# Kernel tuning notes

Measured on AMD Instinct MI355X. Metric: run time of the kernel, lower is better.

The kernel has to match this reference:

```python
import jax, jax.numpy as jnp
import numpy as np

NUM_HEADS = 16
HEAD_DIM = 64
ROT_DIM = 64
NUM_EXPERTS = 8
TOP_K = 2
EPS = 1e-6


def _rms_norm(x, w):
    var = jnp.mean(x * x, axis=-1, keepdims=True)
    return w * x * jax.lax.rsqrt(var + EPS)


def _rotate_half(x):
    h = x.shape[-1] // 2
    return jnp.concatenate((-x[..., h:], x[..., :h]), axis=-1)


def _rotary_cos_sin(seq_len, rot_dim, dtype):
    inv_freq = 1.0 / (10000.0 ** (jnp.arange(0, rot_dim, 2, dtype=jnp.float32) / rot_dim))
    t = jnp.arange(seq_len, dtype=jnp.float32)
    freqs = t[:, None] * inv_freq[None, :]            # [S, rot/2]
    emb = jnp.concatenate((freqs, freqs), axis=-1)    # [S, rot]
    return jnp.cos(emb).astype(dtype), jnp.sin(emb).astype(dtype)


def setup_inputs() -> dict:
    key = jax.random.key(0)
    ks = jax.random.split(key, 10)
    B, S, D, H, E = 2, 2048, 1024, 2048, NUM_EXPERTS
    s = lambda fan: 1.0 / np.sqrt(fan)
    return {
        "x": jax.random.normal(ks[0], (B, S, D), jnp.float32),
        "norm1_w": jnp.ones((D,), jnp.float32),
        "norm2_w": jnp.ones((D,), jnp.float32),
        "qkv_w": jax.random.normal(ks[1], (3 * D, D), jnp.float32) * s(D),
        "qkv_b": jnp.zeros((3 * D,), jnp.float32),
        "out_w": jax.random.normal(ks[2], (D, D), jnp.float32) * s(D),
        "out_b": jnp.zeros((D,), jnp.float32),
        "gate_w": jax.random.normal(ks[3], (E, D), jnp.float32) * s(D),
        "w1": jax.random.normal(ks[4], (E, H, D), jnp.float32) * s(D),
        "b1": jnp.zeros((E, H), jnp.float32),
        "w2": jax.random.normal(ks[5], (E, H, D), jnp.float32) * s(D),
        "b2": jnp.zeros((E, H), jnp.float32),
        "w3": jax.random.normal(ks[6], (E, D, H), jnp.float32) * s(H),
        "b3": jnp.zeros((E, D), jnp.float32),
    }


def _attention(x, qkv_w, qkv_b, out_w, out_b):
    B, S, D = x.shape
    qkv = x @ qkv_w.T + qkv_b                                  # [B,S,3D]
    qkv = qkv.reshape(B, S, 3, NUM_HEADS, HEAD_DIM)
    qkv = jnp.transpose(qkv, (2, 0, 3, 1, 4))                  # [3,B,H,S,Dh]
    q, k, v = qkv[0], qkv[1], qkv[2]
    cos, sin = _rotary_cos_sin(S, ROT_DIM, x.dtype)            # [S,rot]
    cos = cos[None, None]
    sin = sin[None, None]

    def rope(t):
        tr = t[..., :ROT_DIM]
        return jnp.concatenate((tr * cos + _rotate_half(tr) * sin, t[..., ROT_DIM:]), axis=-1)

    q, k = rope(q), rope(k)
    scale = HEAD_DIM ** -0.5
    scores = jnp.einsum("bhqd,bhkd->bhqk", q, k) * scale
    attn = jax.nn.softmax(scores, axis=-1)
    out = jnp.einsum("bhqk,bhkd->bhqd", attn, v)
    out = jnp.transpose(out, (0, 2, 1, 3)).reshape(B, S, D)
    return out @ out_w.T + out_b


def _sparse_moe(x, gate_w, w1, b1, w2, b2, w3, b3):
    logits = x @ gate_w.T                                      # [B,S,E]
    top_vals, top_idx = jax.lax.top_k(logits, TOP_K)
    gate_scores = jax.nn.softmax(top_vals, axis=-1)            # [B,S,k]
    # combined per-expert weight [B,S,E]
    comb = jnp.sum(jax.nn.one_hot(top_idx, NUM_EXPERTS, dtype=x.dtype)
                   * gate_scores[..., None], axis=-2)
    out = jnp.zeros_like(x)
    for e in range(NUM_EXPERTS):  # small fixed expert count; matches dense all-expert compute
        h = jax.nn.silu(x @ w1[e].T + b1[e]) * (x @ w2[e].T + b2[e])
        y = h @ w3[e].T + b3[e]
        out = out + y * comb[..., e:e + 1]
    return out


def reference(x, norm1_w, norm2_w, qkv_w, qkv_b, out_w, out_b,
              gate_w, w1, b1, w2, b2, w3, b3):
    x = x + _attention(_rms_norm(x, norm1_w), qkv_w, qkv_b, out_w, out_b)
    x = x + _sparse_moe(_rms_norm(x, norm2_w), gate_w, w1, b1, w2, b2, w3, b3)
    return x
```

## Files before the change

### kernel.cpp

```cpp
#include <hip/hip_runtime.h>
#include <stdint.h>

typedef unsigned short u16;
typedef __attribute__((ext_vector_type(4))) float f32x4;
typedef __attribute__((ext_vector_type(8))) short bf16x8;

#define MFMA16(a, b, c) __builtin_amdgcn_mfma_f32_16x16x32_bf16((a), (b), (c), 0, 0, 0)

__device__ __forceinline__ float bu2f(u16 u) {
  union { unsigned int i; float f; } c; c.i = ((unsigned int)u) << 16; return c.f;
}
__device__ __forceinline__ u16 f2bu(float f) {
  union { float f; unsigned int i; } c; c.f = f;
  unsigned int x = c.i;
  return (u16)((x + 0x7FFFu + ((x >> 16) & 1u)) >> 16);
}

typedef const __attribute__((address_space(1))) void GVoid;
typedef __attribute__((address_space(3))) void LVoid;

__device__ __forceinline__ void gl_lds16(const void* g, void* l) {
  __builtin_amdgcn_global_load_lds((GVoid*)(uintptr_t)g, (LVoid*)(uintptr_t)l, 16, 0, 0);
}

struct __align__(16) bf8pack { u16 v[8]; };
struct __align__(8) bf4pack { u16 v[4]; };

__global__ __launch_bounds__(256) void f2b_kernel(const float* __restrict__ in,
                                                  u16* __restrict__ out, int n8) {
  int i = blockIdx.x * 256 + threadIdx.x;
  if (i >= n8) return;
  const f32x4* in4 = (const f32x4*)in;
  f32x4 a = in4[i * 2], b = in4[i * 2 + 1];
  bf8pack p;
  p.v[0] = f2bu(a[0]); p.v[1] = f2bu(a[1]); p.v[2] = f2bu(a[2]); p.v[3] = f2bu(a[3]);
  p.v[4] = f2bu(b[0]); p.v[5] = f2bu(b[1]); p.v[6] = f2bu(b[2]); p.v[7] = f2bu(b[3]);
  ((bf8pack*)out)[i] = p;
}

__global__ __launch_bounds__(256) void wsplit3_kernel(const float* __restrict__ w,
                                                      u16* __restrict__ out) {
  int i = blockIdx.x * 256 + threadIdx.x;
  int n = i >> 7, k0 = (i & 127) * 8;
  const f32x4* p = (const f32x4*)(w + (size_t)n * 1024 + k0);
  f32x4 a = p[0], b = p[1];
  float f[8] = {a[0], a[1], a[2], a[3], b[0], b[1], b[2], b[3]};
  bf8pack hi, lo;
#pragma unroll
  for (int t = 0; t < 8; ++t) {
    hi.v[t] = f2bu(f[t]);
    lo.v[t] = f2bu(f[t] - bu2f(hi.v[t]));
  }
  u16* o = out + (size_t)n * 3072 + k0;
  *(bf8pack*)o = hi;
  *(bf8pack*)(o + 1024) = hi;
  *(bf8pack*)(o + 2048) = lo;
}

__global__ __launch_bounds__(256) void asplit3_kernel(const float* __restrict__ a,
                                                      u16* __restrict__ out) {
  int i = blockIdx.x * 256 + threadIdx.x;
  int n = i >> 7, k0 = (i & 127) * 8;
  const f32x4* p = (const f32x4*)(a + (size_t)n * 1024 + k0);
  f32x4 x = p[0], y = p[1];
  float f[8] = {x[0], x[1], x[2], x[3], y[0], y[1], y[2], y[3]};
  bf8pack hi, lo;
#pragma unroll
  for (int t = 0; t < 8; ++t) {
    hi.v[t] = f2bu(f[t]);
    lo.v[t] = f2bu(f[t] - bu2f(hi.v[t]));
  }
  u16* o = out + (size_t)n * 3072 + k0;
  *(bf8pack*)o = hi;
  *(bf8pack*)(o + 1024) = lo;
  *(bf8pack*)(o + 2048) = hi;
}

__global__ __launch_bounds__(256) void rmsnorm3_kernel(const float* __restrict__ x,
                                                       const float* __restrict__ w,
                                                       u16* __restrict__ out) {
  int row = blockIdx.x;
  int tid = threadIdx.x;
  const f32x4* xr = (const f32x4*)(x + (size_t)row * 1024);
  f32x4 v = xr[tid];
  float ss = v[0] * v[0] + v[1] * v[1] + v[2] * v[2] + v[3] * v[3];
#pragma unroll
  for (int off = 32; off; off >>= 1) ss += __shfl_xor(ss, off);
  __shared__ float part[4];
  if ((tid & 63) == 0) part[tid >> 6] = ss;
  __syncthreads();
  float rs = rsqrtf((part[0] + part[1] + part[2] + part[3]) * (1.0f / 1024.0f) + 1e-6f);
  const f32x4* w4 = (const f32x4*)w;
  f32x4 wv = w4[tid];
  float f[4] = {v[0] * rs * wv[0], v[1] * rs * wv[1], v[2] * rs * wv[2], v[3] * rs * wv[3]};
  bf4pack hi, lo;
#pragma unroll
  for (int t = 0; t < 4; ++t) {
    hi.v[t] = f2bu(f[t]);
    lo.v[t] = f2bu(f[t] - bu2f(hi.v[t]));
  }
  u16* o = out + (size_t)row * 3072;
  ((bf4pack*)o)[tid] = hi;
  ((bf4pack*)(o + 1024))[tid] = lo;
  ((bf4pack*)(o + 2048))[tid] = hi;
}

__global__ __launch_bounds__(256) void rmsnorm_kernel(const float* __restrict__ x,
                                                      const float* __restrict__ w,
                                                      u16* __restrict__ out) {
  int row = blockIdx.x;
  int tid = threadIdx.x;
  const f32x4* xr = (const f32x4*)(x + (size_t)row * 1024);
  f32x4 v = xr[tid];
  float ss = v[0] * v[0] + v[1] * v[1] + v[2] * v[2] + v[3] * v[3];
#pragma unroll
  for (int off = 32; off; off >>= 1) ss += __shfl_xor(ss, off);
  __shared__ float part[4];
  if ((tid & 63) == 0) part[tid >> 6] = ss;
  __syncthreads();
  float rs = rsqrtf((part[0] + part[1] + part[2] + part[3]) * (1.0f / 1024.0f) + 1e-6f);
  const f32x4* w4 = (const f32x4*)w;
  f32x4 wv = w4[tid];
  bf4pack o;
  o.v[0] = f2bu(v[0] * rs * wv[0]);
  o.v[1] = f2bu(v[1] * rs * wv[1]);
  o.v[2] = f2bu(v[2] * rs * wv[2]);
  o.v[3] = f2bu(v[3] * rs * wv[3]);
  ((bf4pack*)out)[(size_t)row * 256 + tid] = o;
}

template <int MODE>
__global__ __launch_bounds__(256, 2) void gemm_kernel(
    const u16* __restrict__ A, const u16* __restrict__ B1g, const u16* __restrict__ B2g,
    const float* __restrict__ bias1, const float* __restrict__ bias2,
    void* __restrict__ outp, const float* __restrict__ resid, int N, int K,
    const int* __restrict__ counts, const int* __restrict__ opad,
    const int* __restrict__ slot_token, const float* __restrict__ slot_weight) {
  constexpr bool DUAL = (MODE == 2);
  const int tid = threadIdx.x;
  const int lane = tid & 63;
  const int wid = tid >> 6;
  const int wr = wid >> 1, wc = wid & 1;
  const int n0 = blockIdx.x * 128;
  const int mt = blockIdx.y;
  const int e = (MODE >= 2) ? blockIdx.z : 0;
  int m0;
  if (MODE >= 2) {
    int cnt = counts[e];
    if (mt * 128 >= cnt) return;
    m0 = opad[e] + mt * 128;
  } else {
    m0 = mt * 128;
  }
  const u16* B1 = B1g + ((MODE >= 2) ? (size_t)e * (size_t)N * (size_t)K : (size_t)0);
  const u16* B2 = DUAL ? (B2g + (size_t)e * (size_t)N * (size_t)K) : nullptr;
  const float* bb1 = bias1 + ((MODE >= 2) ? e * N : 0);
  const float* bb2 = DUAL ? (bias2 + e * N) : nullptr;

  __shared__ u16 smem[(DUAL ? 3 : 2) * 128 * 64];
  u16* As = smem;
  u16* Bs = smem + 128 * 64;
  u16* B2s = smem + 2 * 128 * 64;

  const f32x4 zero4 = {0.f, 0.f, 0.f, 0.f};
  f32x4 acc[4][4], acc2[4][4];
#pragma unroll
  for (int mi = 0; mi < 4; ++mi)
#pragma unroll
    for (int ni = 0; ni < 4; ++ni) {
      acc[mi][ni] = zero4;
      if constexpr (DUAL) acc2[mi][ni] = zero4;
    }

  const int rsel = lane & 15;
  const int ksel = lane >> 4;

  for (int k0 = 0; k0 < K; k0 += 64) {
    if (k0) __syncthreads();
#pragma unroll
    for (int i = 0; i < 4; ++i) {
      int c = tid + i * 256;
      int row = c >> 3;
      int col = (c & 7) * 8;
      size_t arow;
      if constexpr (MODE == 2) arow = (size_t)slot_token[m0 + row];
      else arow = (size_t)(m0 + row);
      gl_lds16(A + arow * (size_t)K + k0 + col, As + c * 8);
      gl_lds16(B1 + (size_t)(n0 + row) * K + k0 + col, Bs + c * 8);
      if constexpr (DUAL) gl_lds16(B2 + (size_t)(n0 + row) * K + k0 + col, B2s + c * 8);
    }
    __syncthreads();
    const u16* Aw = As + (wr * 64) * 64;
    const u16* Bw = Bs + (wc * 64) * 64;
    const u16* B2w = B2s + (wc * 64) * 64;
#pragma unroll
    for (int ks = 0; ks < 2; ++ks) {
      int ko = ks * 32 + ksel * 8;
      bf16x8 a[4], b[4];
#pragma unroll
      for (int mi = 0; mi < 4; ++mi) a[mi] = *(const bf16x8*)(Aw + (mi * 16 + rsel) * 64 + ko);
#pragma unroll
      for (int ni = 0; ni < 4; ++ni) b[ni] = *(const bf16x8*)(Bw + (ni * 16 + rsel) * 64 + ko);
#pragma unroll
      for (int mi = 0; mi < 4; ++mi)
#pragma unroll
        for (int ni = 0; ni < 4; ++ni) acc[mi][ni] = MFMA16(a[mi], b[ni], acc[mi][ni]);
      if constexpr (DUAL) {
        bf16x8 b2[4];
#pragma unroll
        for (int ni = 0; ni < 4; ++ni) b2[ni] = *(const bf16x8*)(B2w + (ni * 16 + rsel) * 64 + ko);
#pragma unroll
        for (int mi = 0; mi < 4; ++mi)
#pragma unroll
          for (int ni = 0; ni < 4; ++ni) acc2[mi][ni] = MFMA16(a[mi], b2[ni], acc2[mi][ni]);
      }
    }
  }

#pragma unroll
  for (int mi = 0; mi < 4; ++mi) {
#pragma unroll
    for (int j = 0; j < 4; ++j) {
      int gm = m0 + wr * 64 + mi * 16 + ksel * 4 + j;
#pragma unroll
      for (int ni = 0; ni < 4; ++ni) {
        int gn = n0 + wc * 64 + ni * 16 + rsel;
        float v = acc[mi][ni][j];
        if constexpr (MODE == 0) {
          ((float*)outp)[(size_t)gm * N + gn] = v + bb1[gn];
        } else if constexpr (MODE == 1) {
          ((float*)outp)[(size_t)gm * N + gn] = v + bb1[gn] + resid[(size_t)gm * N + gn];
        } else if constexpr (MODE == 2) {
          float v1 = v + bb1[gn];
          float v2 = acc2[mi][ni][j] + bb2[gn];
          float hv = (v1 / (1.f + __expf(-v1))) * v2;
          ((u16*)outp)[(size_t)gm * N + gn] = f2bu(hv);
        } else {
          int tok = slot_token[gm];
          float w = slot_weight[gm];
          atomicAdd(((float*)outp) + (size_t)tok * N + gn, (v + bb1[gn]) * w);
        }
      }
    }
  }
}

__global__ __launch_bounds__(256) void rope_split_kernel(
    const float* __restrict__ qkv, u16* __restrict__ qhp, u16* __restrict__ qlp,
    u16* __restrict__ khp, u16* __restrict__ klp, u16* __restrict__ vhp,
    u16* __restrict__ vlp) {
  int idx = blockIdx.x * 256 + threadIdx.x;
  int hd = idx & 63;
  int s = (idx >> 6) & 2047;
  int bh = idx >> 17;
  int b = bh >> 4, h = bh & 15;
  size_t base = (size_t)(b * 2048 + s) * 3072 + (size_t)h * 64;
  float qv = qkv[base + hd];
  float qp = qkv[base + (hd ^ 32)];
  float kv = qkv[base + 1024 + hd];
  float kp = qkv[base + 1024 + (hd ^ 32)];
  float vv = qkv[base + 2048 + hd];
  int j = hd & 31;
  double invf = exp((double)j * (-9.210340371976184 / 32.0));
  double ang = (double)s * invf;
  const double twopi = 6.283185307179586;
  double r = ang - twopi * floor(ang / twopi);
  float sn, c;
  sincosf((float)r, &sn, &c);
  float qo = (hd < 32) ? (qv * c - qp * sn) : (qv * c + qp * sn);
  float ko = (hd < 32) ? (kv * c - kp * sn) : (kv * c + kp * sn);
  u16 qh = f2bu(qo), kh = f2bu(ko), vh = f2bu(vv);
  qhp[idx] = qh; qlp[idx] = f2bu(qo - bu2f(qh));
  khp[idx] = kh; klp[idx] = f2bu(ko - bu2f(kh));
  vhp[idx] = vh; vlp[idx] = f2bu(vv - bu2f(vh));
}

__global__ __launch_bounds__(256, 2) void flash_kernel(
    const u16* __restrict__ qhp, const u16* __restrict__ qlp, const u16* __restrict__ khp,
    const u16* __restrict__ klp, const u16* __restrict__ vhp, const u16* __restrict__ vlp,
    float* __restrict__ attn_out) {
  int qblk = blockIdx.x, bh = blockIdx.y;
  int tid = threadIdx.x, lane = tid & 63, wid = tid >> 6;
  const int rsel = lane & 15, ksel = lane >> 4;
  const size_t bhbase = (size_t)bh * 2048 * 64;
  __shared__ u16 Ksh[64 * 64], Ksl[64 * 64];
  __shared__ u16 Vsh[64 * 64], Vsl[64 * 64];
  __shared__ u16 Psh[4][16 * 64], Psl[4][16 * 64];
  int qr0 = qblk * 64 + wid * 16;
  bf16x8 qfh[2], qfl[2];
#pragma unroll
  for (int ks = 0; ks < 2; ++ks) {
    size_t qoff = bhbase + (size_t)(qr0 + rsel) * 64 + ks * 32 + ksel * 8;
    qfh[ks] = *(const bf16x8*)(qhp + qoff);
    qfl[ks] = *(const bf16x8*)(qlp + qoff);
  }

  const f32x4 zero4 = {0.f, 0.f, 0.f, 0.f};
  f32x4 po[4];
  float m_i[4], l_i[4];
#pragma unroll
  for (int i = 0; i < 4; ++i) { po[i] = zero4; m_i[i] = -1e30f; l_i[i] = 0.f; }

  for (int kv0 = 0; kv0 < 2048; kv0 += 64) {
    __syncthreads();
#pragma unroll
    for (int i = 0; i < 2; ++i) {
      int c = tid + i * 256;
      gl_lds16(khp + bhbase + (size_t)kv0 * 64 + c * 8, Ksh + c * 8);
      gl_lds16(klp + bhbase + (size_t)kv0 * 64 + c * 8, Ksl + c * 8);
    }
#pragma unroll
    for (int i = 0; i < 2; ++i) {
      int c = tid + i * 256;
      int r = c >> 3, col0 = (c & 7) * 8;
      bf16x8 a = *(const bf16x8*)(vhp + bhbase + (size_t)(kv0 + r) * 64 + col0);
      bf16x8 bl = *(const bf16x8*)(vlp + bhbase + (size_t)(kv0 + r) * 64 + col0);
#pragma unroll
      for (int jj = 0; jj < 8; ++jj) {
        Vsh[(col0 + jj) * 64 + r] = (u16)a[jj];
        Vsl[(col0 + jj) * 64 + r] = (u16)bl[jj];
      }
    }
    __syncthreads();

    f32x4 sa[4] = {zero4, zero4, zero4, zero4};
#pragma unroll
    for (int ks = 0; ks < 2; ++ks) {
      int ko = ks * 32 + ksel * 8;
#pragma unroll
      for (int ni = 0; ni < 4; ++ni) {
        bf16x8 kbh = *(const bf16x8*)(Ksh + (ni * 16 + rsel) * 64 + ko);
        bf16x8 kbl = *(const bf16x8*)(Ksl + (ni * 16 + rsel) * 64 + ko);
        sa[ni] = MFMA16(qfh[ks], kbh, sa[ni]);
        sa[ni] = MFMA16(qfl[ks], kbh, sa[ni]);
        sa[ni] = MFMA16(qfh[ks], kbl, sa[ni]);
      }
    }
    const float scale = 0.125f;
    float corr[4];
#pragma unroll
    for (int i = 0; i < 4; ++i) {
      float t = sa[0][i] * scale;
      t = fmaxf(t, sa[1][i] * scale);
      t = fmaxf(t, sa[2][i] * scale);
      t = fmaxf(t, sa[3][i] * scale);
#pragma unroll
      for (int off = 1; off < 16; off <<= 1) t = fmaxf(t, __shfl_xor(t, off));
      float mn = fmaxf(m_i[i], t);
      corr[i] = __expf(m_i[i] - mn);
      m_i[i] = mn;
    }
    float rsum[4] = {0.f, 0.f, 0.f, 0.f};
#pragma unroll
    for (int ni = 0; ni < 4; ++ni)
#pragma unroll
      for (int i = 0; i < 4; ++i) {
        float p = __expf(sa[ni][i] * scale - m_i[i]);
        rsum[i] += p;
        u16 ph = f2bu(p);
        Psh[wid][(ksel * 4 + i) * 64 + ni * 16 + rsel] = ph;
        Psl[wid][(ksel * 4 + i) * 64 + ni * 16 + rsel] = f2bu(p - bu2f(ph));
      }
#pragma unroll
    for (int i = 0; i < 4; ++i) {
      float t = rsum[i];
#pragma unroll
      for (int off = 1; off < 16; off <<= 1) t += __shfl_xor(t, off);
      l_i[i] = l_i[i] * corr[i] + t;
    }
#pragma unroll
    for (int nh = 0; nh < 4; ++nh)
#pragma unroll
      for (int i = 0; i < 4; ++i) po[nh][i] *= corr[i];
    __syncthreads();
#pragma unroll
    for (int ks = 0; ks < 2; ++ks) {
      int ko = ks * 32 + ksel * 8;
      bf16x8 pfh = *(const bf16x8*)(&Psh[wid][rsel * 64 + ko]);
      bf16x8 pfl = *(const bf16x8*)(&Psl[wid][rsel * 64 + ko]);
#pragma unroll
      for (int nh = 0; nh < 4; ++nh) {
        bf16x8 vbh = *(const bf16x8*)(Vsh + (nh * 16 + rsel) * 64 + ko);
        bf16x8 vbl = *(const bf16x8*)(Vsl + (nh * 16 + rsel) * 64 + ko);
        po[nh] = MFMA16(pfh, vbh, po[nh]);
        po[nh] = MFMA16(pfl, vbh, po[nh]);
        po[nh] = MFMA16(pfh, vbl, po[nh]);
      }
    }
  }
  int b = bh >> 4, h = bh & 15;
#pragma unroll
  for (int i = 0; i < 4; ++i) {
    float inv = 1.0f / l_i[i];
    int row = qr0 + ksel * 4 + i;
    size_t obase = (size_t)(b * 2048 + row) * 1024 + (size_t)h * 64;
#pragma unroll
    for (int nh = 0; nh < 4; ++nh) attn_out[obase + nh * 16 + rsel] = po[nh][i] * inv;
  }
}

__global__ __launch_bounds__(256) void gate_kernel(const float* __restrict__ xres,
                                                   const float* __restrict__ n2w,
                                                   const float* __restrict__ gw,
                                                   int* __restrict__ tok_e, float* __restrict__ tok_w,
                                                   int* __restrict__ counts) {
  int token = blockIdx.x * 4 + (threadIdx.x >> 6);
  int lane = threadIdx.x & 63;
  const f32x4* xr = (const f32x4*)(xres + (size_t)token * 1024);
  f32x4 xv[4];
  float ss = 0.f;
#pragma unroll
  for (int i = 0; i < 4; ++i) {
    xv[i] = xr[lane * 4 + i];
    ss += xv[i][0] * xv[i][0] + xv[i][1] * xv[i][1] + xv[i][2] * xv[i][2] + xv[i][3] * xv[i][3];
  }
#pragma unroll
  for (int off = 32; off; off >>= 1) ss += __shfl_xor(ss, off);
  float rs = rsqrtf(ss * (1.0f / 1024.0f) + 1e-6f);
  const f32x4* w4 = (const f32x4*)n2w;
#pragma unroll
  for (int i = 0; i < 4; ++i) {
    f32x4 wv = w4[lane * 4 + i];
    xv[i][0] *= rs * wv[0]; xv[i][1] *= rs * wv[1]; xv[i][2] *= rs * wv[2]; xv[i][3] *= rs * wv[3];
  }
  float lg[8];
#pragma unroll
  for (int ee = 0; ee < 8; ++ee) {
    const f32x4* g4 = (const f32x4*)(gw + ee * 1024);
    float a = 0.f;
#pragma unroll
    for (int i = 0; i < 4; ++i) {
      f32x4 g = g4[lane * 4 + i];
      a += xv[i][0] * g[0] + xv[i][1] * g[1] + xv[i][2] * g[2] + xv[i][3] * g[3];
    }
#pragma unroll
    for (int off = 32; off; off >>= 1) a += __shfl_xor(a, off);
    lg[ee] = a;
  }
  if (lane == 0) {
    int i1 = 0; float v1 = lg[0];
#pragma unroll
    for (int ee = 1; ee < 8; ++ee) if (lg[ee] > v1) { v1 = lg[ee]; i1 = ee; }
    int i2 = -1; float v2 = -3e38f;
#pragma unroll
    for (int ee = 0; ee < 8; ++ee) if (ee != i1 && lg[ee] > v2) { v2 = lg[ee]; i2 = ee; }
    float s2 = 1.f / (1.f + __expf(v1 - v2));
    float s1 = 1.f - s2;
    tok_e[token * 2] = i1; tok_e[token * 2 + 1] = i2;
    tok_w[token * 2] = s1; tok_w[token * 2 + 1] = s2;
    atomicAdd(&counts[i1], 1); atomicAdd(&counts[i2], 1);
  }
}

__global__ void init_kernel(int* counts, int* cursor, int* slot_token, float* slot_weight) {
  int i = blockIdx.x * 256 + threadIdx.x;
  if (i < 8) { counts[i] = 0; cursor[i] = 0; }
  if (i < 10240) { slot_token[i] = 0; slot_weight[i] = 0.f; }
}

__global__ void scan_kernel(const int* counts, int* opad) {
  if (threadIdx.x == 0) {
    int off = 0;
    for (int e = 0; e < 8; ++e) { opad[e] = off; off += ((counts[e] + 127) >> 7) << 7; }
  }
}

__global__ __launch_bounds__(256) void assign_kernel(const int* __restrict__ tok_e,
                                                     const float* __restrict__ tok_w,
                                                     const int* __restrict__ opad, int* cursor,
                                                     int* __restrict__ slot_token,
                                                     float* __restrict__ slot_weight) {
  int t = blockIdx.x * 256 + threadIdx.x;
#pragma unroll
  for (int j = 0; j < 2; ++j) {
    int e = tok_e[t * 2 + j];
    int pos = atomicAdd(&cursor[e], 1);
    slot_token[opad[e] + pos] = t;
    slot_weight[opad[e] + pos] = tok_w[t * 2 + j];
  }
}

extern "C" void kernel_launch(void* const* d_in, const int* in_sizes, int n_in, void* d_out,
                              int out_size, void* d_ws, size_t ws_size, hipStream_t stream) {
  const float* x = (const float*)d_in[0];
  const float* n1w = (const float*)d_in[1];
  const float* n2w = (const float*)d_in[2];
  const float* qkv_w = (const float*)d_in[3];
  const float* qkv_b = (const float*)d_in[4];
  const float* out_w = (const float*)d_in[5];
  const float* out_b = (const float*)d_in[6];
  const float* gate_w = (const float*)d_in[7];
  const float* w1 = (const float*)d_in[8];
  const float* b1 = (const float*)d_in[9];
  const float* w2 = (const float*)d_in[10];
  const float* b2 = (const float*)d_in[11];
  const float* w3 = (const float*)d_in[12];
  const float* b3 = (const float*)d_in[13];
  float* out = (float*)d_out;

  const size_t MB = 1024 * 1024;
  char* ws = (char*)d_ws;
  char* R0 = ws;
  char* R1 = ws + 96 * MB;
  char* R2 = R1 + 44 * MB;
  char* R3 = R2 + 16 * MB;
  char* R4 = R3 + 8 * MB;
  if ((size_t)(165 * MB) > ws_size) return;

  float* qkvbuf = (float*)R0;
  u16* qhp = (u16*)(R0 + 48 * MB);
  u16* qlp = (u16*)(R0 + 56 * MB);
  u16* khp = (u16*)(R0 + 64 * MB);
  u16* klp = (u16*)(R0 + 72 * MB);
  u16* vhp = (u16*)(R0 + 80 * MB);
  u16* vlp = (u16*)(R0 + 88 * MB);
  u16* w1b = (u16*)R0;
  u16* w2b = (u16*)(R0 + 32 * MB);
  u16* w3b = (u16*)(R0 + 64 * MB);
  u16* xn3 = (u16*)R1;
  u16* qkvw3 = (u16*)(R1 + 24 * MB);
  u16* attn3 = (u16*)R1;
  u16* hbuf = (u16*)R1;
  float* attnout = (float*)R2;
  u16* xn_moe = (u16*)R2;
  u16* outw3 = (u16*)R3;
  int* tok_e = (int*)R4;
  float* tok_w = (float*)(R4 + 64 * 1024);
  int* counts = (int*)(R4 + 128 * 1024);
  int* cursor = (int*)(R4 + 132 * 1024);
  int* opad = (int*)(R4 + 136 * 1024);
  int* slot_token = (int*)(R4 + 192 * 1024);
  float* slot_weight = (float*)(R4 + 256 * 1024);

  rmsnorm3_kernel<<<4096, 256, 0, stream>>>(x, n1w, xn3);
  wsplit3_kernel<<<1536, 256, 0, stream>>>(qkv_w, qkvw3);
  wsplit3_kernel<<<512, 256, 0, stream>>>(out_w, outw3);
  gemm_kernel<0><<<dim3(24, 32, 1), 256, 0, stream>>>(xn3, qkvw3, nullptr, qkv_b, nullptr, qkvbuf,
                                                      nullptr, 3072, 3072, nullptr, nullptr,
                                                      nullptr, nullptr);
  rope_split_kernel<<<16384, 256, 0, stream>>>(qkvbuf, qhp, qlp, khp, klp, vhp, vlp);
  flash_kernel<<<dim3(32, 32, 1), 256, 0, stream>>>(qhp, qlp, khp, klp, vhp, vlp, attnout);
  f2b_kernel<<<8192, 256, 0, stream>>>(w1, w1b, 2097152);
  f2b_kernel<<<8192, 256, 0, stream>>>(w2, w2b, 2097152);
  f2b_kernel<<<8192, 256, 0, stream>>>(w3, w3b, 2097152);
  asplit3_kernel<<<2048, 256, 0, stream>>>(attnout, attn3);
  gemm_kernel<1><<<dim3(8, 32, 1), 256, 0, stream>>>(attn3, outw3, nullptr, out_b, nullptr, out, x,
                                                     1024, 3072, nullptr, nullptr, nullptr, nullptr);
  rmsnorm_kernel<<<4096, 256, 0, stream>>>(out, n2w, xn_moe);
  init_kernel<<<40, 256, 0, stream>>>(counts, cursor, slot_token, slot_weight);
  gate_kernel<<<1024, 256, 0, stream>>>(out, n2w, gate_w, tok_e, tok_w, counts);
  scan_kernel<<<1, 64, 0, stream>>>(counts, opad);
  assign_kernel<<<16, 256, 0, stream>>>(tok_e, tok_w, opad, cursor, slot_token, slot_weight);
  gemm_kernel<2><<<dim3(16, 32, 8), 256, 0, stream>>>(xn_moe, w1b, w2b, b1, b2, hbuf, nullptr, 2048,
                                                      1024, counts, opad, slot_token, slot_weight);
  gemm_kernel<3><<<dim3(8, 32, 8), 256, 0, stream>>>(hbuf, w3b, nullptr, b3, nullptr, out, nullptr,
                                                     1024, 2048, counts, opad, slot_token,
                                                     slot_weight);
}
```

Measured before the change: 1.170 ms.

## Swizzle flash-attention LDS tiles, raise occupancy, and prioritize MFMA sections

Applies an XOR swizzle to the K, V and P shared-memory tiles in the flash attention kernel so the 16-byte fragment reads and transposed V writes avoid LDS bank conflicts. K tiles loaded through global_load_lds are swizzled on the source address, so each LDS slot holds the element its read index expects. It also raises the launch bound to 3 blocks per SM and wraps the MFMA loops in s_setprio. The extra occupancy may cause register spills, and the swizzle adds index arithmetic to every access.

```diff
diff --git a/kernel.cpp b/kernel.cpp
--- a/kernel.cpp
+++ b/kernel.cpp
@@ -22,6 +22,8 @@
 __device__ __forceinline__ void gl_lds16(const void* g, void* l) {
   __builtin_amdgcn_global_load_lds((GVoid*)(uintptr_t)g, (LVoid*)(uintptr_t)l, 16, 0, 0);
 }
+
+__device__ __forceinline__ int swz(int row) { return ((row ^ (row >> 3)) & 7) << 3; }
 
 struct __align__(16) bf8pack { u16 v[8]; };
 struct __align__(8) bf4pack { u16 v[4]; };
@@ -275,7 +277,7 @@
   vhp[idx] = vh; vlp[idx] = f2bu(vv - bu2f(vh));
 }
 
-__global__ __launch_bounds__(256, 2) void flash_kernel(
+__global__ __launch_bounds__(256, 3) void flash_kernel(
     const u16* __restrict__ qhp, const u16* __restrict__ qlp, const u16* __restrict__ khp,
     const u16* __restrict__ klp, const u16* __restrict__ vhp, const u16* __restrict__ vlp,
     float* __restrict__ attn_out) {
@@ -306,8 +308,9 @@
 #pragma unroll
     for (int i = 0; i < 2; ++i) {
       int c = tid + i * 256;
-      gl_lds16(khp + bhbase + (size_t)kv0 * 64 + c * 8, Ksh + c * 8);
-      gl_lds16(klp + bhbase + (size_t)kv0 * 64 + c * 8, Ksl + c * 8);
+      int srcoff = (c * 8) ^ swz(c >> 3);
+      gl_lds16(khp + bhbase + (size_t)kv0 * 64 + srcoff, Ksh + c * 8);
+      gl_lds16(klp + bhbase + (size_t)kv0 * 64 + srcoff, Ksl + c * 8);
     }
 #pragma unroll
     for (int i = 0; i < 2; ++i) {
@@ -317,25 +320,31 @@
       bf16x8 bl = *(const bf16x8*)(vlp + bhbase + (size_t)(kv0 + r) * 64 + col0);
 #pragma unroll
       for (int jj = 0; jj < 8; ++jj) {
-        Vsh[(col0 + jj) * 64 + r] = (u16)a[jj];
-        Vsl[(col0 + jj) * 64 + r] = (u16)bl[jj];
+        int d = col0 + jj;
+        int widx = (d * 64 + r) ^ swz(d);
+        Vsh[widx] = (u16)a[jj];
+        Vsl[widx] = (u16)bl[jj];
       }
     }
     __syncthreads();
 
     f32x4 sa[4] = {zero4, zero4, zero4, zero4};
+    __builtin_amdgcn_s_setprio(1);
 #pragma unroll
     for (int ks = 0; ks < 2; ++ks) {
       int ko = ks * 32 + ksel * 8;
 #pragma unroll
       for (int ni = 0; ni < 4; ++ni) {
-        bf16x8 kbh = *(const bf16x8*)(Ksh + (ni * 16 + rsel) * 64 + ko);
-        bf16x8 kbl = *(const bf16x8*)(Ksl + (ni * 16 + rsel) * 64 + ko);
+        int row = ni * 16 + rsel;
+        int idx = (row * 64 + ko) ^ swz(row);
+        bf16x8 kbh = *(const bf16x8*)(Ksh + idx);
+        bf16x8 kbl = *(const bf16x8*)(Ksl + idx);
         sa[ni] = MFMA16(qfh[ks], kbh, sa[ni]);
         sa[ni] = MFMA16(qfl[ks], kbh, sa[ni]);
         sa[ni] = MFMA16(qfh[ks], kbl, sa[ni]);
       }
     }
+    __builtin_amdgcn_s_setprio(0);
     const float scale = 0.125f;
     float corr[4];
 #pragma unroll
@@ -358,8 +367,10 @@
         float p = __expf(sa[ni][i] * scale - m_i[i]);
         rsum[i] += p;
         u16 ph = f2bu(p);
-        Psh[wid][(ksel * 4 + i) * 64 + ni * 16 + rsel] = ph;
-        Psl[wid][(ksel * 4 + i) * 64 + ni * 16 + rsel] = f2bu(p - bu2f(ph));
+        int prow = ksel * 4 + i;
+        int pidx = (prow * 64 + ni * 16 + rsel) ^ swz(prow);
+        Psh[wid][pidx] = ph;
+        Psl[wid][pidx] = f2bu(p - bu2f(ph));
       }
 #pragma unroll
     for (int i = 0; i < 4; ++i) {
@@ -373,20 +384,25 @@
 #pragma unroll
       for (int i = 0; i < 4; ++i) po[nh][i] *= corr[i];
     __syncthreads();
+    __builtin_amdgcn_s_setprio(1);
 #pragma unroll
     for (int ks = 0; ks < 2; ++ks) {
       int ko = ks * 32 + ksel * 8;
-      bf16x8 pfh = *(const bf16x8*)(&Psh[wid][rsel * 64 + ko]);
-      bf16x8 pfl = *(const bf16x8*)(&Psl[wid][rsel * 64 + ko]);
+      int pidx = (rsel * 64 + ko) ^ swz(rsel);
+      bf16x8 pfh = *(const bf16x8*)(&Psh[wid][pidx]);
+      bf16x8 pfl = *(const bf16x8*)(&Psl[wid][pidx]);
 #pragma unroll
       for (int nh = 0; nh < 4; ++nh) {
-        bf16x8 vbh = *(const bf16x8*)(Vsh + (nh * 16 + rsel) * 64 + ko);
-        bf16x8 vbl = *(const bf16x8*)(Vsl + (nh * 16 + rsel) * 64 + ko);
+        int row = nh * 16 + rsel;
+        int idx = (row * 64 + ko) ^ swz(row);
+        bf16x8 vbh = *(const bf16x8*)(Vsh + idx);
+        bf16x8 vbl = *(const bf16x8*)(Vsl + idx);
         po[nh] = MFMA16(pfh, vbh, po[nh]);
         po[nh] = MFMA16(pfl, vbh, po[nh]);
         po[nh] = MFMA16(pfh, vbl, po[nh]);
       }
     }
+    __builtin_amdgcn_s_setprio(0);
   }
   int b = bh >> 4, h = bh & 15;
 #pragma unroll
```

New measurement: 1.089 ms. -6.9%, faster.
